# Kernel tuning notes

Hardware: AMD Instinct MI355X
Metric: run time of the kernel (lower is better)

## Reference

```python
import jax, jax.numpy as jnp
import numpy as np
from jax import lax


def linear_recurrence(decays, impulses):
    """s[t] = decays[t]*s[t-1] + impulses[t], s[-1]=0, via associative scan over axis 0."""
    def comb(e1, e2):
        a1, b1 = e1
        a2, b2 = e2
        return a2 * a1, a2 * b1 + b2
    return lax.associative_scan(comb, (decays, impulses), axis=0)[1]


def setup_inputs() -> dict:
    key = jax.random.key(0)
    ks = jax.random.split(key, 6)
    b, T, d = 16, 1024, 128
    n, m, k = 64, 128, 16
    x = jax.random.normal(ks[0], (b, T, d), jnp.float32)
    R = jax.random.normal(ks[1], (d, k), jnp.float32)               # fixed projection
    theta = jax.random.uniform(ks[2], (k, n // 2), jnp.float32, -np.pi, np.pi)  # eig angles
    C = jax.random.uniform(ks[3], (k, m, n), jnp.float32, -1e-6, 1e-6) / n
    D = jax.random.uniform(ks[4], (k, m), jnp.float32, -1e-3, 1e-3)
    Do = jax.random.uniform(ks[5], (m,), jnp.float32, -1e-7, 1e-7)
    return {"x": x, "R": R, "theta": theta, "C": C, "D": D, "Do": Do}


def _ldstack(x, R, theta, C, D, Do, Delta=2, standard=True):
    c64 = jnp.complex64
    b, T, d = x.shape
    k, half = theta.shape
    n = 2 * half
    m = C.shape[1]
    # (b,T,d) -> (T,b,d) complex, project d -> k
    xc = jnp.transpose(x, (1, 0, 2)).astype(c64) @ R.astype(c64)  # (T,b,k)
    # unitary eigenvalues: lnλ = i*[θ, -θ]
    lnlam = (1j * jnp.concatenate([theta, -theta], axis=1)).astype(c64)  # (k,n)
    lam = jnp.exp(lnlam)
    # B' coefficients (log-space product over eigenvalue ratios, diag excluded)
    eye = jnp.eye(n, dtype=bool)
    ratios = jnp.where(eye[None], 0.0, lam[:, :, None] / lam[:, None, :])  # (k,n,n)
    B = jnp.exp(-jnp.sum(jnp.log(1.0 - ratios), axis=1))                    # (k,n)
    # C' coefficients: C'[k,j,m] = sum_i C[k,m,i] * λ[k,j]^{-(n-i)}
    powers = (n - jnp.arange(1, n + 1)).astype(c64)           # (n,) = [n-1,...,0]
    U = jnp.exp(-powers[None, :, None] * lnlam[:, None, :])   # (k,i,j)
    Cp = jnp.einsum('kmi,kij->kjm', C.astype(c64), U)         # (k,n,m)
    Dc = D.astype(c64)
    Doc = Do.astype(c64)

    alpha = None
    y = None
    for _ in range(Delta):
        Bx = (xc[..., None] * B).reshape(T, b, k * n)          # (T,b,k*n)
        if alpha is None:
            al = jnp.broadcast_to(lam.reshape(1, 1, k * n), (T, b, k * n))
        else:
            al = (alpha * lam).reshape(T, b, k * n)
        if standard:
            z = jnp.zeros((1, b, k * n), c64)
            al = jnp.concatenate([z, al[:-1]], axis=0)
            Bx = jnp.concatenate([z, Bx[:-1]], axis=0)
        s = linear_recurrence(al, Bx).reshape(T, b, k, n)      # (T,b,k,n)
        y = (jnp.einsum('tbkn,knm->tbkm', s, Cp)
             + xc[..., None] * Dc[None, None]
             + Doc)                                            # (T,b,k,m)
        ls = lam[None, None] * s
        alpha = (1.0 / jnp.sqrt(1.0 + jnp.abs(ls) ** 2)).astype(c64)  # recipsq
    y = jnp.mean(y, axis=2).real                               # (T,b,m)
    return jnp.transpose(y, (1, 0, 2))                         # (b,T,m)


def reference(x, R, theta, C, D, Do):
    return _ldstack(x, R, theta, C, D, Do, Delta=2, standard=True)
```

## Files before the change

kernel.cpp:

```cpp
#include <hip/hip_runtime.h>
#include <math.h>

#define TLEN 1024
#define BSZ  16
#define DIN  128
#define KP   16
#define NEIG 64
#define MOUT 128
#define CHUNK_T 256
#define NCHUNK  4

static constexpr size_t XCQ_OFF = 0;
static constexpr size_t LAM_OFF = 262144;
static constexpr size_t BQ_OFF  = 264192;
static constexpr size_t CP_OFF  = 266240;
static constexpr size_t ST_OFF  = 528384;
static constexpr size_t S2_OFF  = 593920;
static constexpr size_t P_OFF   = 8982528;

__device__ __forceinline__ float f32cos(float x) { return (float)cos((double)x); }
__device__ __forceinline__ float f32sin(float x) { return (float)sin((double)x); }

__device__ __forceinline__ float2 cdiv32(float ar, float ai, float cr, float ci) {
  float2 o;
  if (fabsf(ci) <= fabsf(cr)) {
    float rat = __fdiv_rn(ci, cr);
    float scl = __fdiv_rn(1.0f, __fadd_rn(cr, __fmul_rn(ci, rat)));
    o.x = __fmul_rn(__fadd_rn(ar, __fmul_rn(ai, rat)), scl);
    o.y = __fmul_rn(__fsub_rn(ai, __fmul_rn(ar, rat)), scl);
  } else {
    float rat = __fdiv_rn(cr, ci);
    float scl = __fdiv_rn(1.0f, __fadd_rn(ci, __fmul_rn(cr, rat)));
    o.x = __fmul_rn(__fadd_rn(__fmul_rn(ar, rat), ai), scl);
    o.y = __fmul_rn(__fsub_rn(__fmul_rn(ai, rat), ar), scl);
  }
  return o;
}

__global__ __launch_bounds__(256) void k_lam_B(const float* __restrict__ theta,
                        float2* __restrict__ lam, float2* __restrict__ Bq) {
  __shared__ float2 terms[4][64];
  int wid  = threadIdx.x >> 6;
  int lane = threadIdx.x & 63;
  int idx = blockIdx.x * 4 + wid;
  int k = idx >> 6, j = idx & 63;
  float thj = (j < 32) ? theta[k * 32 + j] : -theta[k * 32 + (j - 32)];
  float ljr = f32cos(thj), lji = f32sin(thj);
  float2 tm = make_float2(0.f, 0.f);
  if (lane != j) {
    int i = lane;
    float thi = (i < 32) ? theta[k * 32 + i] : -theta[k * 32 + (i - 32)];
    float lir = f32cos(thi), lii = f32sin(thi);
    float2 r = cdiv32(lir, lii, ljr, lji);
    float tr = __fsub_rn(1.0f, r.x);
    float ti = __fsub_rn(0.0f, r.y);
    double h = sqrt((double)tr * tr + (double)ti * ti);
    tm.x = (float)log(h);
    tm.y = (float)atan2((double)ti, (double)tr);
  }
  terms[wid][lane] = tm;
  __syncthreads();
  if (lane == 0) {
    lam[idx] = make_float2(ljr, lji);
    float sr = 0.f, si = 0.f;
    for (int i = 0; i < NEIG; ++i) {
      sr = __fadd_rn(sr, terms[wid][i].x);
      si = __fadd_rn(si, terms[wid][i].y);
    }
    float er = (float)exp((double)(-sr));
    float cc = f32cos(-si), ss = f32sin(-si);
    Bq[idx] = make_float2(__fmul_rn(er, cc), __fmul_rn(er, ss));
  }
}

__global__ __launch_bounds__(128) void k_Cp(const float* __restrict__ theta,
                     const float* __restrict__ C, float2* __restrict__ Cp) {
  __shared__ float2 sU[64];
  __shared__ float  sC[128][65];
  int tid = threadIdx.x;
  int kj = blockIdx.x;
  int j = kj & 63, k = kj >> 6;
  float lnim = (j < 32) ? theta[k * 32 + j] : -theta[k * 32 + (j - 32)];
  if (tid < 64) {
    int i = tid;
    float p = (float)(63 - i);
    float ph = -__fmul_rn(p, lnim);
    sU[i] = make_float2(f32cos(ph), f32sin(ph));
  }
  const float* Ck = C + ((size_t)k << 13);
  for (int e = tid; e < 128 * 64; e += 128) {
    sC[e >> 6][e & 63] = Ck[e];
  }
  __syncthreads();
  int m = tid;
  float ar = 0.f, ai = 0.f;
  #pragma unroll 8
  for (int i = 0; i < NEIG; ++i) {
    float Cv = sC[m][i];
    float2 U = sU[i];
    ar = __fadd_rn(ar, __fmul_rn(Cv, U.x));
    ai = __fadd_rn(ai, __fmul_rn(Cv, U.y));
  }
  Cp[(size_t)(k * 64 + j) * MOUT + m] = make_float2(ar, ai);
}

__global__ __launch_bounds__(256) void k_xc(const float* __restrict__ x,
                     const float* __restrict__ R, float* __restrict__ xcq) {
  __shared__ float sX[16][132];
  __shared__ float sR[128][16];
  int tid = threadIdx.x;
  int rBase = blockIdx.x * 16;
  for (int e = tid; e < DIN * KP; e += 256) sR[e >> 4][e & 15] = R[e];
  #pragma unroll
  for (int it = 0; it < 2; ++it) {
    int e = tid + it * 256;
    int row = e >> 5, q = e & 31;
    int g = rBase + row;
    int t = g >> 4, b = g & 15;
    float4 v = *(const float4*)(x + ((size_t)b * TLEN + t) * DIN + q * 4);
    *(float4*)&sX[row][q * 4] = v;
  }
  __syncthreads();
  int r = tid >> 4, k = tid & 15;
  double acc = 0.0;
  #pragma unroll 16
  for (int d = 0; d < DIN; ++d)
    acc = fma((double)sX[r][d], (double)sR[d][k], acc);
  xcq[(size_t)(rBase + r) * KP + k] = (float)acc;
}

__global__ __launch_bounds__(64) void k_scan(const float2* __restrict__ lam,
                        const float2* __restrict__ Bq,
                        const float* __restrict__ xcq,
                        float2* __restrict__ S2,
                        float* __restrict__ state, int c) {
  __shared__ float sXq[CHUNK_T];
  int j = threadIdx.x;
  int chain = blockIdx.x;
  int b = chain >> 4, k = chain & 15;
  int mode = k * 64 + j;
  int t0 = c * CHUNK_T;
  int tlBeg = (c == 0) ? 1 : 0;
  for (int i = j; i < CHUNK_T; i += 64) {
    int g = t0 + tlBeg - 1 + i;
    sXq[i] = xcq[(size_t)g * (BSZ * KP) + b * KP + k];
  }
  __syncthreads();
  float lr = lam[mode].x, li = lam[mode].y;
  float Br = Bq[mode].x,  Bi = Bq[mode].y;
  float* st = state + (size_t)(chain * 64 + j) * 4;
  float s1r, s1i, s2r, s2i;
  if (c == 0) { s1r = s1i = s2r = s2i = 0.f; }
  else        { s1r = st[0]; s1i = st[1]; s2r = st[2]; s2i = st[3]; }
  float lsr = __fsub_rn(__fmul_rn(lr, s1r), __fmul_rn(li, s1i));
  float lsi = __fadd_rn(__fmul_rn(lr, s1i), __fmul_rn(li, s1r));
  float h  = (float)sqrt((double)lsr * lsr + (double)lsi * lsi);
  float al = __fdiv_rn(1.0f, __fsqrt_rn(__fadd_rn(1.0f, __fmul_rn(h, h))));
  if (c == 0)
    S2[(size_t)(0 * BSZ + b) * 1024 + mode] = make_float2(s2r, s2i);
  #pragma unroll 4
  for (int tl = tlBeg; tl < CHUNK_T; ++tl) {
    float xq = sXq[tl - tlBeg];
    float bxr = __fmul_rn(xq, Br), bxi = __fmul_rn(xq, Bi);
    float a2r = __fmul_rn(al, lr), a2i = __fmul_rn(al, li);
    float t2r = __fsub_rn(__fmul_rn(a2r, s2r), __fmul_rn(a2i, s2i));
    float t2i = __fadd_rn(__fmul_rn(a2r, s2i), __fmul_rn(a2i, s2r));
    s2r = __fadd_rn(t2r, bxr);
    s2i = __fadd_rn(t2i, bxi);
    s1r = __fadd_rn(lsr, bxr);
    s1i = __fadd_rn(lsi, bxi);
    lsr = __fsub_rn(__fmul_rn(lr, s1r), __fmul_rn(li, s1i));
    lsi = __fadd_rn(__fmul_rn(lr, s1i), __fmul_rn(li, s1r));
    h  = (float)sqrt((double)lsr * lsr + (double)lsi * lsi);
    al = __fdiv_rn(1.0f, __fsqrt_rn(__fadd_rn(1.0f, __fmul_rn(h, h))));
    S2[(size_t)(tl * BSZ + b) * 1024 + mode] = make_float2(s2r, s2i);
  }
  st[0] = s1r; st[1] = s1i; st[2] = s2r; st[3] = s2i;
}

__global__ __launch_bounds__(256, 2) void k_y(const float2* __restrict__ S2,
                     const float2* __restrict__ Cp, const float* __restrict__ xcq,
                     const float* __restrict__ D, const float* __restrict__ Dov,
                     float* __restrict__ P, int c) {
  __shared__ float2 sS2t[32][129];
  __shared__ float2 sCp[32][128];
  int tid = threadIdx.x;
  int kidx = blockIdx.x >> 5;
  int rt   = blockIdx.x & 31;
  int rowBase = rt * 128;
  int rg = tid & 15;
  int cg = tid >> 4;
  int c0 = cg * 8;
  float acc[8][8];
  #pragma unroll
  for (int jj = 0; jj < 8; ++jj)
    #pragma unroll
    for (int q = 0; q < 8; ++q) acc[jj][q] = 0.f;

  #pragma unroll 1
  for (int nh = 0; nh < 2; ++nh) {
    __syncthreads();
    #pragma unroll
    for (int it = 0; it < 8; ++it) {
      int e = tid + it * 256;
      int n2 = (e & 15) * 2;
      int row = e >> 4;
      float4 v = *(const float4*)(S2 + (size_t)(rowBase + row) * 1024
                                     + kidx * 64 + nh * 32 + n2);
      sS2t[n2][row]     = make_float2(v.x, v.y);
      sS2t[n2 + 1][row] = make_float2(v.z, v.w);
    }
    #pragma unroll
    for (int it = 0; it < 8; ++it) {
      int e = tid + it * 256;
      int col2 = (e & 63) * 2;
      int n = e >> 6;
      float4 v = *(const float4*)(Cp + (size_t)(kidx * 64 + nh * 32 + n) * MOUT + col2);
      *(float4*)&sCp[n][col2] = v;
    }
    __syncthreads();
    #pragma unroll 2
    for (int n = 0; n < 32; ++n) {
      float2 a[8];
      #pragma unroll
      for (int jj = 0; jj < 8; ++jj) a[jj] = sS2t[n][rg + jj * 16];
      float4 w[4];
      #pragma unroll
      for (int q = 0; q < 4; ++q) w[q] = *(const float4*)&sCp[n][c0 + q * 2];
      float cx[8] = {w[0].x, w[0].z, w[1].x, w[1].z, w[2].x, w[2].z, w[3].x, w[3].z};
      float cy[8] = {w[0].y, w[0].w, w[1].y, w[1].w, w[2].y, w[2].w, w[3].y, w[3].w};
      #pragma unroll
      for (int jj = 0; jj < 8; ++jj)
        #pragma unroll
        for (int q = 0; q < 8; ++q)
          acc[jj][q] = __fadd_rn(acc[jj][q],
              __fsub_rn(__fmul_rn(a[jj].x, cx[q]), __fmul_rn(a[jj].y, cy[q])));
    }
  }
  float dv[8], ovv[8];
  *(float4*)&dv[0]  = *(const float4*)(D + kidx * MOUT + c0);
  *(float4*)&dv[4]  = *(const float4*)(D + kidx * MOUT + c0 + 4);
  *(float4*)&ovv[0] = *(const float4*)(Dov + c0);
  *(float4*)&ovv[4] = *(const float4*)(Dov + c0 + 4);
  #pragma unroll
  for (int jj = 0; jj < 8; ++jj) {
    int row = rowBase + rg + jj * 16;
    float xv = xcq[(size_t)(c * 4096 + row) * KP + kidx];
    float res[8];
    #pragma unroll
    for (int q = 0; q < 8; ++q)
      res[q] = __fadd_rn(__fadd_rn(acc[jj][q], __fmul_rn(xv, dv[q])), ovv[q]);
    float* pp = P + ((size_t)kidx * 4096 + row) * MOUT + c0;
    *(float4*)pp       = make_float4(res[0], res[1], res[2], res[3]);
    *(float4*)(pp + 4) = make_float4(res[4], res[5], res[6], res[7]);
  }
}

__global__ __launch_bounds__(256) void k_combine(const float* __restrict__ P,
                     float* __restrict__ out, int c) {
  int idx = blockIdx.x * 256 + threadIdx.x;
  int r  = idx >> 5;
  int m4 = (idx & 31) * 4;
  float4 s = *(const float4*)(P + (size_t)r * MOUT + m4);
  #pragma unroll
  for (int k = 1; k < KP; ++k) {
    float4 p = *(const float4*)(P + ((size_t)k * 4096 + r) * MOUT + m4);
    s.x = __fadd_rn(s.x, p.x);
    s.y = __fadd_rn(s.y, p.y);
    s.z = __fadd_rn(s.z, p.z);
    s.w = __fadd_rn(s.w, p.w);
  }
  int rg = c * 4096 + r;
  int t = rg >> 4, b = rg & 15;
  float4 res;
  res.x = __fdiv_rn(s.x, 16.0f);
  res.y = __fdiv_rn(s.y, 16.0f);
  res.z = __fdiv_rn(s.z, 16.0f);
  res.w = __fdiv_rn(s.w, 16.0f);
  *(float4*)(out + ((size_t)b * TLEN + t) * MOUT + m4) = res;
}

extern "C" void kernel_launch(void* const* d_in, const int* in_sizes, int n_in,
                              void* d_out, int out_size, void* d_ws, size_t ws_size,
                              hipStream_t stream) {
  const float* x     = (const float*)d_in[0];
  const float* R     = (const float*)d_in[1];
  const float* theta = (const float*)d_in[2];
  const float* C     = (const float*)d_in[3];
  const float* D     = (const float*)d_in[4];
  const float* Do    = (const float*)d_in[5];
  float* out = (float*)d_out;
  float* ws  = (float*)d_ws;
  float*  xcq = ws + XCQ_OFF;
  float2* lam = (float2*)(ws + LAM_OFF);
  float2* Bq  = (float2*)(ws + BQ_OFF);
  float2* Cp  = (float2*)(ws + CP_OFF);
  float*  st  = ws + ST_OFF;
  float2* S2  = (float2*)(ws + S2_OFF);
  float*  P   = ws + P_OFF;

  hipLaunchKernelGGL(k_lam_B, dim3(256),  dim3(256), 0, stream, theta, lam, Bq);
  hipLaunchKernelGGL(k_Cp,    dim3(1024), dim3(128), 0, stream, theta, C, Cp);
  hipLaunchKernelGGL(k_xc,    dim3(1024), dim3(256), 0, stream, x, R, xcq);
  for (int c = 0; c < NCHUNK; ++c) {
    hipLaunchKernelGGL(k_scan,    dim3(256), dim3(64),  0, stream, lam, Bq, xcq, S2, st, c);
    hipLaunchKernelGGL(k_y,       dim3(512), dim3(256), 0, stream, S2, Cp, xcq, D, Do, P, c);
    hipLaunchKernelGGL(k_combine, dim3(512), dim3(256), 0, stream, P, out, c);
  }
}
```

Baseline: 379.8 us.

## Split scan into two passes via shared alpha buffer and retile k_y smaller

The scan kernel now computes the first-pass recurrence and the per-step alpha normalisation in one loop and stores alpha in shared memory. A second loop then runs the second-pass recurrence reading those alphas. This takes the expensive double-precision sqrt and fp32 divide off the serial dependency chain of the second recurrence, at the cost of 64KB of LDS per block and two sequential passes. Separately, k_y is retiled to 128-thread blocks over 64 rows with 16-mode slices, which doubles the grid and uses interleaved column access.

```diff
diff --git a/kernel.cpp b/kernel.cpp
--- a/kernel.cpp
+++ b/kernel.cpp
@@ -135,6 +135,7 @@
                         float2* __restrict__ S2,
                         float* __restrict__ state, int c) {
   __shared__ float sXq[CHUNK_T];
+  __shared__ float sAl[CHUNK_T * 64];
   int j = threadIdx.x;
   int chain = blockIdx.x;
   int b = chain >> 4, k = chain & 15;
@@ -152,45 +153,50 @@
   float s1r, s1i, s2r, s2i;
   if (c == 0) { s1r = s1i = s2r = s2i = 0.f; }
   else        { s1r = st[0]; s1i = st[1]; s2r = st[2]; s2i = st[3]; }
-  float lsr = __fsub_rn(__fmul_rn(lr, s1r), __fmul_rn(li, s1i));
-  float lsi = __fadd_rn(__fmul_rn(lr, s1i), __fmul_rn(li, s1r));
-  float h  = (float)sqrt((double)lsr * lsr + (double)lsi * lsi);
-  float al = __fdiv_rn(1.0f, __fsqrt_rn(__fadd_rn(1.0f, __fmul_rn(h, h))));
+
+  #pragma unroll 4
+  for (int tl = tlBeg; tl < CHUNK_T; ++tl) {
+    float xq = sXq[tl - tlBeg];
+    float lsr = __fsub_rn(__fmul_rn(lr, s1r), __fmul_rn(li, s1i));
+    float lsi = __fadd_rn(__fmul_rn(lr, s1i), __fmul_rn(li, s1r));
+    float h  = (float)sqrt((double)lsr * lsr + (double)lsi * lsi);
+    float al = __fdiv_rn(1.0f, __fsqrt_rn(__fadd_rn(1.0f, __fmul_rn(h, h))));
+    sAl[tl * 64 + j] = al;
+    float bxr = __fmul_rn(xq, Br), bxi = __fmul_rn(xq, Bi);
+    s1r = __fadd_rn(lsr, bxr);
+    s1i = __fadd_rn(lsi, bxi);
+  }
+  __syncthreads();
+
   if (c == 0)
     S2[(size_t)(0 * BSZ + b) * 1024 + mode] = make_float2(s2r, s2i);
   #pragma unroll 4
   for (int tl = tlBeg; tl < CHUNK_T; ++tl) {
     float xq = sXq[tl - tlBeg];
+    float al = sAl[tl * 64 + j];
     float bxr = __fmul_rn(xq, Br), bxi = __fmul_rn(xq, Bi);
     float a2r = __fmul_rn(al, lr), a2i = __fmul_rn(al, li);
     float t2r = __fsub_rn(__fmul_rn(a2r, s2r), __fmul_rn(a2i, s2i));
     float t2i = __fadd_rn(__fmul_rn(a2r, s2i), __fmul_rn(a2i, s2r));
     s2r = __fadd_rn(t2r, bxr);
     s2i = __fadd_rn(t2i, bxi);
-    s1r = __fadd_rn(lsr, bxr);
-    s1i = __fadd_rn(lsi, bxi);
-    lsr = __fsub_rn(__fmul_rn(lr, s1r), __fmul_rn(li, s1i));
-    lsi = __fadd_rn(__fmul_rn(lr, s1i), __fmul_rn(li, s1r));
-    h  = (float)sqrt((double)lsr * lsr + (double)lsi * lsi);
-    al = __fdiv_rn(1.0f, __fsqrt_rn(__fadd_rn(1.0f, __fmul_rn(h, h))));
     S2[(size_t)(tl * BSZ + b) * 1024 + mode] = make_float2(s2r, s2i);
   }
   st[0] = s1r; st[1] = s1i; st[2] = s2r; st[3] = s2i;
 }
 
-__global__ __launch_bounds__(256, 2) void k_y(const float2* __restrict__ S2,
+__global__ __launch_bounds__(128, 2) void k_y(const float2* __restrict__ S2,
                      const float2* __restrict__ Cp, const float* __restrict__ xcq,
                      const float* __restrict__ D, const float* __restrict__ Dov,
                      float* __restrict__ P, int c) {
-  __shared__ float2 sS2t[32][129];
-  __shared__ float2 sCp[32][128];
+  __shared__ float2 sS2t[16][65];
+  __shared__ float2 sCp[16][128];
   int tid = threadIdx.x;
-  int kidx = blockIdx.x >> 5;
-  int rt   = blockIdx.x & 31;
-  int rowBase = rt * 128;
-  int rg = tid & 15;
-  int cg = tid >> 4;
-  int c0 = cg * 8;
+  int kidx = blockIdx.x >> 6;
+  int rt   = blockIdx.x & 63;
+  int rowBase = rt * 64;
+  int rg = tid & 7;
+  int cg = tid >> 3;
   float acc[8][8];
   #pragma unroll
   for (int jj = 0; jj < 8; ++jj)
@@ -198,61 +204,66 @@
     for (int q = 0; q < 8; ++q) acc[jj][q] = 0.f;
 
   #pragma unroll 1
-  for (int nh = 0; nh < 2; ++nh) {
+  for (int nh = 0; nh < 4; ++nh) {
     __syncthreads();
     #pragma unroll
-    for (int it = 0; it < 8; ++it) {
-      int e = tid + it * 256;
-      int n2 = (e & 15) * 2;
-      int row = e >> 4;
+    for (int it = 0; it < 4; ++it) {
+      int e = tid + it * 128;
+      int n2 = (e & 7) * 2;
+      int row = e >> 3;
       float4 v = *(const float4*)(S2 + (size_t)(rowBase + row) * 1024
-                                     + kidx * 64 + nh * 32 + n2);
+                                     + kidx * 64 + nh * 16 + n2);
       sS2t[n2][row]     = make_float2(v.x, v.y);
       sS2t[n2 + 1][row] = make_float2(v.z, v.w);
     }
     #pragma unroll
     for (int it = 0; it < 8; ++it) {
-      int e = tid + it * 256;
+      int e = tid + it * 128;
       int col2 = (e & 63) * 2;
       int n = e >> 6;
-      float4 v = *(const float4*)(Cp + (size_t)(kidx * 64 + nh * 32 + n) * MOUT + col2);
+      float4 v = *(const float4*)(Cp + (size_t)(kidx * 64 + nh * 16 + n) * MOUT + col2);
       *(float4*)&sCp[n][col2] = v;
     }
     __syncthreads();
-    #pragma unroll 2
-    for (int n = 0; n < 32; ++n) {
+    #pragma unroll 4
+    for (int n = 0; n < 16; ++n) {
       float2 a[8];
       #pragma unroll
-      for (int jj = 0; jj < 8; ++jj) a[jj] = sS2t[n][rg + jj * 16];
+      for (int jj = 0; jj < 8; ++jj) a[jj] = sS2t[n][rg + jj * 8];
       float4 w[4];
       #pragma unroll
-      for (int q = 0; q < 4; ++q) w[q] = *(const float4*)&sCp[n][c0 + q * 2];
-      float cx[8] = {w[0].x, w[0].z, w[1].x, w[1].z, w[2].x, w[2].z, w[3].x, w[3].z};
-      float cy[8] = {w[0].y, w[0].w, w[1].y, w[1].w, w[2].y, w[2].w, w[3].y, w[3].w};
+      for (int q = 0; q < 4; ++q) w[q] = *(const float4*)&sCp[n][cg * 2 + q * 32];
       #pragma unroll
       for (int jj = 0; jj < 8; ++jj)
         #pragma unroll
-        for (int q = 0; q < 8; ++q)
-          acc[jj][q] = __fadd_rn(acc[jj][q],
-              __fsub_rn(__fmul_rn(a[jj].x, cx[q]), __fmul_rn(a[jj].y, cy[q])));
+        for (int q = 0; q < 4; ++q) {
+          acc[jj][2 * q]     = __fadd_rn(acc[jj][2 * q],
+              __fsub_rn(__fmul_rn(a[jj].x, w[q].x), __fmul_rn(a[jj].y, w[q].y)));
+          acc[jj][2 * q + 1] = __fadd_rn(acc[jj][2 * q + 1],
+              __fsub_rn(__fmul_rn(a[jj].x, w[q].z), __fmul_rn(a[jj].y, w[q].w)));
+        }
     }
   }
   float dv[8], ovv[8];
-  *(float4*)&dv[0]  = *(const float4*)(D + kidx * MOUT + c0);
-  *(float4*)&dv[4]  = *(const float4*)(D + kidx * MOUT + c0 + 4);
-  *(float4*)&ovv[0] = *(const float4*)(Dov + c0);
-  *(float4*)&ovv[4] = *(const float4*)(Dov + c0 + 4);
+  #pragma unroll
+  for (int q = 0; q < 4; ++q) {
+    float2 d2 = *(const float2*)(D + kidx * MOUT + cg * 2 + q * 32);
+    float2 o2 = *(const float2*)(Dov + cg * 2 + q * 32);
+    dv[2 * q] = d2.x;  dv[2 * q + 1] = d2.y;
+    ovv[2 * q] = o2.x; ovv[2 * q + 1] = o2.y;
+  }
   #pragma unroll
   for (int jj = 0; jj < 8; ++jj) {
-    int row = rowBase + rg + jj * 16;
+    int row = rowBase + rg + jj * 8;
     float xv = xcq[(size_t)(c * 4096 + row) * KP + kidx];
-    float res[8];
+    float* pp = P + ((size_t)kidx * 4096 + row) * MOUT + cg * 2;
     #pragma unroll
-    for (int q = 0; q < 8; ++q)
-      res[q] = __fadd_rn(__fadd_rn(acc[jj][q], __fmul_rn(xv, dv[q])), ovv[q]);
-    float* pp = P + ((size_t)kidx * 4096 + row) * MOUT + c0;
-    *(float4*)pp       = make_float4(res[0], res[1], res[2], res[3]);
-    *(float4*)(pp + 4) = make_float4(res[4], res[5], res[6], res[7]);
+    for (int q = 0; q < 4; ++q) {
+      float2 r2;
+      r2.x = __fadd_rn(__fadd_rn(acc[jj][2 * q], __fmul_rn(xv, dv[2 * q])), ovv[2 * q]);
+      r2.y = __fadd_rn(__fadd_rn(acc[jj][2 * q + 1], __fmul_rn(xv, dv[2 * q + 1])), ovv[2 * q + 1]);
+      *(float2*)(pp + q * 32) = r2;
+    }
   }
 }
 
@@ -303,8 +314,8 @@
   hipLaunchKernelGGL(k_Cp,    dim3(1024), dim3(128), 0, stream, theta, C, Cp);
   hipLaunchKernelGGL(k_xc,    dim3(1024), dim3(256), 0, stream, x, R, xcq);
   for (int c = 0; c < NCHUNK; ++c) {
-    hipLaunchKernelGGL(k_scan,    dim3(256), dim3(64),  0, stream, lam, Bq, xcq, S2, st, c);
-    hipLaunchKernelGGL(k_y,       dim3(512), dim3(256), 0, stream, S2, Cp, xcq, D, Do, P, c);
-    hipLaunchKernelGGL(k_combine, dim3(512), dim3(256), 0, stream, P, out, c);
-  }
-}
+    hipLaunchKernelGGL(k_scan,    dim3(256),  dim3(64),  0, stream, lam, Bq, xcq, S2, st, c);
+    hipLaunchKernelGGL(k_y,       dim3(1024), dim3(128), 0, stream, S2, Cp, xcq, D, Do, P, c);
+    hipLaunchKernelGGL(k_combine, dim3(512),  dim3(256), 0, stream, P, out, c);
+  }
+}
```

After: 424.0 us. 1.12x slower.

## Split scan into decoupled s1/alpha batches and pack y-GEMM into v2f

Applied to the files above, without the earlier changes.

The per-mode scan loop is split into blocks of 8 steps. The first pass runs the s1 recurrence and computes the alpha values (double-precision sqrt, divide), and the second pass runs the s2 recurrence. This takes the long alpha latency off the s2 dependency chain so independent work can overlap. Separately, the k_y inner product now uses 2-wide float vectors with fp contraction off, so the compiler can emit packed FP32 multiply/add while keeping the same rounding.

```diff
diff --git a/kernel.cpp b/kernel.cpp
--- a/kernel.cpp
+++ b/kernel.cpp
@@ -9,6 +9,8 @@
 #define MOUT 128
 #define CHUNK_T 256
 #define NCHUNK  4
+
+typedef float v2f __attribute__((ext_vector_type(2)));
 
 static constexpr size_t XCQ_OFF = 0;
 static constexpr size_t LAM_OFF = 262144;
@@ -152,15 +154,42 @@
   float s1r, s1i, s2r, s2i;
   if (c == 0) { s1r = s1i = s2r = s2i = 0.f; }
   else        { s1r = st[0]; s1i = st[1]; s2r = st[2]; s2i = st[3]; }
-  float lsr = __fsub_rn(__fmul_rn(lr, s1r), __fmul_rn(li, s1i));
-  float lsi = __fadd_rn(__fmul_rn(lr, s1i), __fmul_rn(li, s1r));
-  float h  = (float)sqrt((double)lsr * lsr + (double)lsi * lsi);
-  float al = __fdiv_rn(1.0f, __fsqrt_rn(__fadd_rn(1.0f, __fmul_rn(h, h))));
   if (c == 0)
     S2[(size_t)(0 * BSZ + b) * 1024 + mode] = make_float2(s2r, s2i);
-  #pragma unroll 4
-  for (int tl = tlBeg; tl < CHUNK_T; ++tl) {
+
+  int tl = tlBeg;
+  for (; tl + 8 <= CHUNK_T; tl += 8) {
+    float als[8];
+    #pragma unroll
+    for (int u = 0; u < 8; ++u) {
+      float xq = sXq[tl - tlBeg + u];
+      float lsr = __fsub_rn(__fmul_rn(lr, s1r), __fmul_rn(li, s1i));
+      float lsi = __fadd_rn(__fmul_rn(lr, s1i), __fmul_rn(li, s1r));
+      float h  = (float)sqrt((double)lsr * lsr + (double)lsi * lsi);
+      als[u] = __fdiv_rn(1.0f, __fsqrt_rn(__fadd_rn(1.0f, __fmul_rn(h, h))));
+      float bxr = __fmul_rn(xq, Br), bxi = __fmul_rn(xq, Bi);
+      s1r = __fadd_rn(lsr, bxr);
+      s1i = __fadd_rn(lsi, bxi);
+    }
+    #pragma unroll
+    for (int u = 0; u < 8; ++u) {
+      float xq = sXq[tl - tlBeg + u];
+      float al = als[u];
+      float bxr = __fmul_rn(xq, Br), bxi = __fmul_rn(xq, Bi);
+      float a2r = __fmul_rn(al, lr), a2i = __fmul_rn(al, li);
+      float t2r = __fsub_rn(__fmul_rn(a2r, s2r), __fmul_rn(a2i, s2i));
+      float t2i = __fadd_rn(__fmul_rn(a2r, s2i), __fmul_rn(a2i, s2r));
+      s2r = __fadd_rn(t2r, bxr);
+      s2i = __fadd_rn(t2i, bxi);
+      S2[(size_t)((tl + u) * BSZ + b) * 1024 + mode] = make_float2(s2r, s2i);
+    }
+  }
+  for (; tl < CHUNK_T; ++tl) {
     float xq = sXq[tl - tlBeg];
+    float lsr = __fsub_rn(__fmul_rn(lr, s1r), __fmul_rn(li, s1i));
+    float lsi = __fadd_rn(__fmul_rn(lr, s1i), __fmul_rn(li, s1r));
+    float h  = (float)sqrt((double)lsr * lsr + (double)lsi * lsi);
+    float al = __fdiv_rn(1.0f, __fsqrt_rn(__fadd_rn(1.0f, __fmul_rn(h, h))));
     float bxr = __fmul_rn(xq, Br), bxi = __fmul_rn(xq, Bi);
     float a2r = __fmul_rn(al, lr), a2i = __fmul_rn(al, li);
     float t2r = __fsub_rn(__fmul_rn(a2r, s2r), __fmul_rn(a2i, s2i));
@@ -169,10 +198,6 @@
     s2i = __fadd_rn(t2i, bxi);
     s1r = __fadd_rn(lsr, bxr);
     s1i = __fadd_rn(lsi, bxi);
-    lsr = __fsub_rn(__fmul_rn(lr, s1r), __fmul_rn(li, s1i));
-    lsi = __fadd_rn(__fmul_rn(lr, s1i), __fmul_rn(li, s1r));
-    h  = (float)sqrt((double)lsr * lsr + (double)lsi * lsi);
-    al = __fdiv_rn(1.0f, __fsqrt_rn(__fadd_rn(1.0f, __fmul_rn(h, h))));
     S2[(size_t)(tl * BSZ + b) * 1024 + mode] = make_float2(s2r, s2i);
   }
   st[0] = s1r; st[1] = s1i; st[2] = s2r; st[3] = s2i;
@@ -182,6 +207,7 @@
                      const float2* __restrict__ Cp, const float* __restrict__ xcq,
                      const float* __restrict__ D, const float* __restrict__ Dov,
                      float* __restrict__ P, int c) {
+#pragma clang fp contract(off)
   __shared__ float2 sS2t[32][129];
   __shared__ float2 sCp[32][128];
   int tid = threadIdx.x;
@@ -191,11 +217,11 @@
   int rg = tid & 15;
   int cg = tid >> 4;
   int c0 = cg * 8;
-  float acc[8][8];
+  v2f acc2[8][4];
   #pragma unroll
   for (int jj = 0; jj < 8; ++jj)
     #pragma unroll
-    for (int q = 0; q < 8; ++q) acc[jj][q] = 0.f;
+    for (int q = 0; q < 4; ++q) acc2[jj][q] = (v2f)(0.f);
 
   #pragma unroll 1
   for (int nh = 0; nh < 2; ++nh) {
@@ -224,17 +250,21 @@
       float2 a[8];
       #pragma unroll
       for (int jj = 0; jj < 8; ++jj) a[jj] = sS2t[n][rg + jj * 16];
-      float4 w[4];
+      v2f wx[4], wy[4];
       #pragma unroll
-      for (int q = 0; q < 4; ++q) w[q] = *(const float4*)&sCp[n][c0 + q * 2];
-      float cx[8] = {w[0].x, w[0].z, w[1].x, w[1].z, w[2].x, w[2].z, w[3].x, w[3].z};
-      float cy[8] = {w[0].y, w[0].w, w[1].y, w[1].w, w[2].y, w[2].w, w[3].y, w[3].w};
+      for (int q = 0; q < 4; ++q) {
+        float4 w = *(const float4*)&sCp[n][c0 + q * 2];
+        wx[q] = (v2f){w.x, w.z};
+        wy[q] = (v2f){w.y, w.w};
+      }
       #pragma unroll
-      for (int jj = 0; jj < 8; ++jj)
+      for (int jj = 0; jj < 8; ++jj) {
+        v2f ax = (v2f)(a[jj].x);
+        v2f ay = (v2f)(a[jj].y);
         #pragma unroll
-        for (int q = 0; q < 8; ++q)
-          acc[jj][q] = __fadd_rn(acc[jj][q],
-              __fsub_rn(__fmul_rn(a[jj].x, cx[q]), __fmul_rn(a[jj].y, cy[q])));
+        for (int q = 0; q < 4; ++q)
+          acc2[jj][q] = acc2[jj][q] + (ax * wx[q] - ay * wy[q]);
+      }
     }
   }
   float dv[8], ovv[8];
@@ -248,8 +278,10 @@
     float xv = xcq[(size_t)(c * 4096 + row) * KP + kidx];
     float res[8];
     #pragma unroll
-    for (int q = 0; q < 8; ++q)
-      res[q] = __fadd_rn(__fadd_rn(acc[jj][q], __fmul_rn(xv, dv[q])), ovv[q]);
+    for (int q = 0; q < 8; ++q) {
+      float accv = (q & 1) ? acc2[jj][q >> 1].y : acc2[jj][q >> 1].x;
+      res[q] = (accv + xv * dv[q]) + ovv[q];
+    }
     float* pp = P + ((size_t)kidx * 4096 + row) * MOUT + c0;
     *(float4*)pp       = make_float4(res[0], res[1], res[2], res[3]);
     *(float4*)(pp + 4) = make_float4(res[4], res[5], res[6], res[7]);
```

New measurement: 406.9 us. 7.1% more time.

## Split scan into two-phase batched loops with two modes per thread; shrink k_y tiles

Applied to the files above, without the earlier changes.

The scan kernel now gives each thread two eigen-modes and lets half the wavefront exit early. Each 8-step block first runs the first-stage recurrence to produce eight alpha values, then runs the second-stage recurrence with them. This is meant to shorten the serial dependency chain and expose more instruction-level parallelism through two independent chains, at the cost of fewer active threads. Separately, k_y stages 16 eigen-modes per shared-memory tile instead of 32 and drops the min-blocks launch bound, which lowers LDS use but adds more sync iterations.

```diff
diff --git a/kernel.cpp b/kernel.cpp
--- a/kernel.cpp
+++ b/kernel.cpp
@@ -138,7 +138,6 @@
   int j = threadIdx.x;
   int chain = blockIdx.x;
   int b = chain >> 4, k = chain & 15;
-  int mode = k * 64 + j;
   int t0 = c * CHUNK_T;
   int tlBeg = (c == 0) ? 1 : 0;
   for (int i = j; i < CHUNK_T; i += 64) {
@@ -146,44 +145,108 @@
     sXq[i] = xcq[(size_t)g * (BSZ * KP) + b * KP + k];
   }
   __syncthreads();
-  float lr = lam[mode].x, li = lam[mode].y;
-  float Br = Bq[mode].x,  Bi = Bq[mode].y;
-  float* st = state + (size_t)(chain * 64 + j) * 4;
-  float s1r, s1i, s2r, s2i;
-  if (c == 0) { s1r = s1i = s2r = s2i = 0.f; }
-  else        { s1r = st[0]; s1i = st[1]; s2r = st[2]; s2i = st[3]; }
-  float lsr = __fsub_rn(__fmul_rn(lr, s1r), __fmul_rn(li, s1i));
-  float lsi = __fadd_rn(__fmul_rn(lr, s1i), __fmul_rn(li, s1r));
-  float h  = (float)sqrt((double)lsr * lsr + (double)lsi * lsi);
-  float al = __fdiv_rn(1.0f, __fsqrt_rn(__fadd_rn(1.0f, __fmul_rn(h, h))));
-  if (c == 0)
-    S2[(size_t)(0 * BSZ + b) * 1024 + mode] = make_float2(s2r, s2i);
-  #pragma unroll 4
-  for (int tl = tlBeg; tl < CHUNK_T; ++tl) {
+  if (j >= 32) return;
+  int m0 = k * 64 + j, m1 = m0 + 32;
+  float lr0 = lam[m0].x, li0 = lam[m0].y, lr1 = lam[m1].x, li1 = lam[m1].y;
+  float Br0 = Bq[m0].x,  Bi0 = Bq[m0].y,  Br1 = Bq[m1].x,  Bi1 = Bq[m1].y;
+  float* st0 = state + (size_t)(chain * 64 + j) * 4;
+  float* st1 = state + (size_t)(chain * 64 + j + 32) * 4;
+  float s1r0, s1i0, s2r0, s2i0, s1r1, s1i1, s2r1, s2i1;
+  if (c == 0) {
+    s1r0 = s1i0 = s2r0 = s2i0 = 0.f;
+    s1r1 = s1i1 = s2r1 = s2i1 = 0.f;
+    S2[(size_t)(0 * BSZ + b) * 1024 + m0] = make_float2(0.f, 0.f);
+    S2[(size_t)(0 * BSZ + b) * 1024 + m1] = make_float2(0.f, 0.f);
+  } else {
+    s1r0 = st0[0]; s1i0 = st0[1]; s2r0 = st0[2]; s2i0 = st0[3];
+    s1r1 = st1[0]; s1i1 = st1[1]; s2r1 = st1[2]; s2i1 = st1[3];
+  }
+
+  int tl = tlBeg;
+  for (; tl + 8 <= CHUNK_T; tl += 8) {
+    float als0[8], als1[8];
+    #pragma unroll
+    for (int u = 0; u < 8; ++u) {
+      float xq = sXq[tl - tlBeg + u];
+      float lsr0 = __fsub_rn(__fmul_rn(lr0, s1r0), __fmul_rn(li0, s1i0));
+      float lsi0 = __fadd_rn(__fmul_rn(lr0, s1i0), __fmul_rn(li0, s1r0));
+      float h0 = (float)sqrt((double)lsr0 * lsr0 + (double)lsi0 * lsi0);
+      als0[u] = __fdiv_rn(1.0f, __fsqrt_rn(__fadd_rn(1.0f, __fmul_rn(h0, h0))));
+      float bxr0 = __fmul_rn(xq, Br0), bxi0 = __fmul_rn(xq, Bi0);
+      s1r0 = __fadd_rn(lsr0, bxr0);
+      s1i0 = __fadd_rn(lsi0, bxi0);
+      float lsr1 = __fsub_rn(__fmul_rn(lr1, s1r1), __fmul_rn(li1, s1i1));
+      float lsi1 = __fadd_rn(__fmul_rn(lr1, s1i1), __fmul_rn(li1, s1r1));
+      float h1 = (float)sqrt((double)lsr1 * lsr1 + (double)lsi1 * lsi1);
+      als1[u] = __fdiv_rn(1.0f, __fsqrt_rn(__fadd_rn(1.0f, __fmul_rn(h1, h1))));
+      float bxr1 = __fmul_rn(xq, Br1), bxi1 = __fmul_rn(xq, Bi1);
+      s1r1 = __fadd_rn(lsr1, bxr1);
+      s1i1 = __fadd_rn(lsi1, bxi1);
+    }
+    #pragma unroll
+    for (int u = 0; u < 8; ++u) {
+      float xq = sXq[tl - tlBeg + u];
+      size_t rowOff = (size_t)((tl + u) * BSZ + b) * 1024;
+      float bxr0 = __fmul_rn(xq, Br0), bxi0 = __fmul_rn(xq, Bi0);
+      float a2r0 = __fmul_rn(als0[u], lr0), a2i0 = __fmul_rn(als0[u], li0);
+      float t2r0 = __fsub_rn(__fmul_rn(a2r0, s2r0), __fmul_rn(a2i0, s2i0));
+      float t2i0 = __fadd_rn(__fmul_rn(a2r0, s2i0), __fmul_rn(a2i0, s2r0));
+      s2r0 = __fadd_rn(t2r0, bxr0);
+      s2i0 = __fadd_rn(t2i0, bxi0);
+      S2[rowOff + m0] = make_float2(s2r0, s2i0);
+      float bxr1 = __fmul_rn(xq, Br1), bxi1 = __fmul_rn(xq, Bi1);
+      float a2r1 = __fmul_rn(als1[u], lr1), a2i1 = __fmul_rn(als1[u], li1);
+      float t2r1 = __fsub_rn(__fmul_rn(a2r1, s2r1), __fmul_rn(a2i1, s2i1));
+      float t2i1 = __fadd_rn(__fmul_rn(a2r1, s2i1), __fmul_rn(a2i1, s2r1));
+      s2r1 = __fadd_rn(t2r1, bxr1);
+      s2i1 = __fadd_rn(t2i1, bxi1);
+      S2[rowOff + m1] = make_float2(s2r1, s2i1);
+    }
+  }
+  for (; tl < CHUNK_T; ++tl) {
     float xq = sXq[tl - tlBeg];
-    float bxr = __fmul_rn(xq, Br), bxi = __fmul_rn(xq, Bi);
-    float a2r = __fmul_rn(al, lr), a2i = __fmul_rn(al, li);
-    float t2r = __fsub_rn(__fmul_rn(a2r, s2r), __fmul_rn(a2i, s2i));
-    float t2i = __fadd_rn(__fmul_rn(a2r, s2i), __fmul_rn(a2i, s2r));
-    s2r = __fadd_rn(t2r, bxr);
-    s2i = __fadd_rn(t2i, bxi);
-    s1r = __fadd_rn(lsr, bxr);
-    s1i = __fadd_rn(lsi, bxi);
-    lsr = __fsub_rn(__fmul_rn(lr, s1r), __fmul_rn(li, s1i));
-    lsi = __fadd_rn(__fmul_rn(lr, s1i), __fmul_rn(li, s1r));
-    h  = (float)sqrt((double)lsr * lsr + (double)lsi * lsi);
-    al = __fdiv_rn(1.0f, __fsqrt_rn(__fadd_rn(1.0f, __fmul_rn(h, h))));
-    S2[(size_t)(tl * BSZ + b) * 1024 + mode] = make_float2(s2r, s2i);
-  }
-  st[0] = s1r; st[1] = s1i; st[2] = s2r; st[3] = s2i;
-}
-
-__global__ __launch_bounds__(256, 2) void k_y(const float2* __restrict__ S2,
+    size_t rowOff = (size_t)(tl * BSZ + b) * 1024;
+    {
+      float lsr = __fsub_rn(__fmul_rn(lr0, s1r0), __fmul_rn(li0, s1i0));
+      float lsi = __fadd_rn(__fmul_rn(lr0, s1i0), __fmul_rn(li0, s1r0));
+      float h  = (float)sqrt((double)lsr * lsr + (double)lsi * lsi);
+      float al = __fdiv_rn(1.0f, __fsqrt_rn(__fadd_rn(1.0f, __fmul_rn(h, h))));
+      float bxr = __fmul_rn(xq, Br0), bxi = __fmul_rn(xq, Bi0);
+      float a2r = __fmul_rn(al, lr0), a2i = __fmul_rn(al, li0);
+      float t2r = __fsub_rn(__fmul_rn(a2r, s2r0), __fmul_rn(a2i, s2i0));
+      float t2i = __fadd_rn(__fmul_rn(a2r, s2i0), __fmul_rn(a2i, s2r0));
+      s2r0 = __fadd_rn(t2r, bxr);
+      s2i0 = __fadd_rn(t2i, bxi);
+      s1r0 = __fadd_rn(lsr, bxr);
+      s1i0 = __fadd_rn(lsi, bxi);
+      S2[rowOff + m0] = make_float2(s2r0, s2i0);
+    }
+    {
+      float lsr = __fsub_rn(__fmul_rn(lr1, s1r1), __fmul_rn(li1, s1i1));
+      float lsi = __fadd_rn(__fmul_rn(lr1, s1i1), __fmul_rn(li1, s1r1));
+      float h  = (float)sqrt((double)lsr * lsr + (double)lsi * lsi);
+      float al = __fdiv_rn(1.0f, __fsqrt_rn(__fadd_rn(1.0f, __fmul_rn(h, h))));
+      float bxr = __fmul_rn(xq, Br1), bxi = __fmul_rn(xq, Bi1);
+      float a2r = __fmul_rn(al, lr1), a2i = __fmul_rn(al, li1);
+      float t2r = __fsub_rn(__fmul_rn(a2r, s2r1), __fmul_rn(a2i, s2i1));
+      float t2i = __fadd_rn(__fmul_rn(a2r, s2i1), __fmul_rn(a2i, s2r1));
+      s2r1 = __fadd_rn(t2r, bxr);
+      s2i1 = __fadd_rn(t2i, bxi);
+      s1r1 = __fadd_rn(lsr, bxr);
+      s1i1 = __fadd_rn(lsi, bxi);
+      S2[rowOff + m1] = make_float2(s2r1, s2i1);
+    }
+  }
+  st0[0] = s1r0; st0[1] = s1i0; st0[2] = s2r0; st0[3] = s2i0;
+  st1[0] = s1r1; st1[1] = s1i1; st1[2] = s2r1; st1[3] = s2i1;
+}
+
+__global__ __launch_bounds__(256) void k_y(const float2* __restrict__ S2,
                      const float2* __restrict__ Cp, const float* __restrict__ xcq,
                      const float* __restrict__ D, const float* __restrict__ Dov,
                      float* __restrict__ P, int c) {
-  __shared__ float2 sS2t[32][129];
-  __shared__ float2 sCp[32][128];
+  __shared__ float2 sS2t[16][129];
+  __shared__ float2 sCp[16][128];
   int tid = threadIdx.x;
   int kidx = blockIdx.x >> 5;
   int rt   = blockIdx.x & 31;
@@ -198,29 +261,29 @@
     for (int q = 0; q < 8; ++q) acc[jj][q] = 0.f;
 
   #pragma unroll 1
-  for (int nh = 0; nh < 2; ++nh) {
+  for (int nh = 0; nh < 4; ++nh) {
     __syncthreads();
     #pragma unroll
-    for (int it = 0; it < 8; ++it) {
+    for (int it = 0; it < 4; ++it) {
       int e = tid + it * 256;
-      int n2 = (e & 15) * 2;
-      int row = e >> 4;
+      int n2 = (e & 7) * 2;
+      int row = e >> 3;
       float4 v = *(const float4*)(S2 + (size_t)(rowBase + row) * 1024
-                                     + kidx * 64 + nh * 32 + n2);
+                                     + kidx * 64 + nh * 16 + n2);
       sS2t[n2][row]     = make_float2(v.x, v.y);
       sS2t[n2 + 1][row] = make_float2(v.z, v.w);
     }
     #pragma unroll
-    for (int it = 0; it < 8; ++it) {
+    for (int it = 0; it < 4; ++it) {
       int e = tid + it * 256;
       int col2 = (e & 63) * 2;
       int n = e >> 6;
-      float4 v = *(const float4*)(Cp + (size_t)(kidx * 64 + nh * 32 + n) * MOUT + col2);
+      float4 v = *(const float4*)(Cp + (size_t)(kidx * 64 + nh * 16 + n) * MOUT + col2);
       *(float4*)&sCp[n][col2] = v;
     }
     __syncthreads();
-    #pragma unroll 2
-    for (int n = 0; n < 32; ++n) {
+    #pragma unroll 4
+    for (int n = 0; n < 16; ++n) {
       float2 a[8];
       #pragma unroll
       for (int jj = 0; jj < 8; ++jj) a[jj] = sS2t[n][rg + jj * 16];
```

Result: slower. 582.0 us (+53.3%).
